# Optimization experiments

Measured on AMD Instinct MI355X. Metric: run time of the kernel, lower is better.

Reference implementation:

```python
import jax, jax.numpy as jnp
import numpy as np

B, T, C, H = 8, 2048, 256, 4
D = C // H  # head_dim = 64
SCALE = D ** -0.5


def setup_inputs() -> dict:
    key = jax.random.key(0)
    ks = jax.random.split(key, 5)
    return {
        "x": jax.random.normal(ks[0], (B, T, C), dtype=jnp.float32),
        "Wqkv": jax.random.normal(ks[1], (C, 3 * C), dtype=jnp.float32) * (C ** -0.5),
        "bqkv": jax.random.normal(ks[2], (3 * C,), dtype=jnp.float32) * 0.02,
        "Wproj": jax.random.normal(ks[3], (C, C), dtype=jnp.float32) * (C ** -0.5),
        "bproj": jax.random.normal(ks[4], (C,), dtype=jnp.float32) * 0.02,
    }


def reference(x, Wqkv, bqkv, Wproj, bproj):
    b, t, c = x.shape
    # QKV projection -> (3, B, H, T, D) matching torch permute(2,0,3,1,4)
    qkv = (x @ Wqkv + bqkv).reshape(b, t, 3, H, D)
    qkv = jnp.transpose(qkv, (2, 0, 3, 1, 4))
    q, k, v = qkv[0], qkv[1], qkv[2]  # each (B, H, T, D)
    # Full T x T scores (faithful to the original non-fused implementation)
    attn = jnp.einsum("bhqd,bhkd->bhqk", q, k) * SCALE
    causal = jnp.triu(jnp.ones((t, t), dtype=bool), k=1)  # True above diagonal
    attn = jnp.where(causal, -jnp.inf, attn)
    attn = jax.nn.softmax(attn, axis=-1)
    # dropout is identity in eval mode
    out = jnp.einsum("bhqk,bhkd->bhqd", attn, v)  # (B, H, T, D)
    out = jnp.transpose(out, (0, 2, 1, 3)).reshape(b, t, c)
    return out @ Wproj + bproj
```

## Files before the change

### kernel.cpp

```cpp
#include <hip/hip_runtime.h>
#include <hip/hip_bf16.h>
#include <math.h>

#define BATCH 8
#define SEQ   2048
#define CH    256
#define NH    4
#define HD    64
#define NQB   (SEQ / 64)
#define SCALE 0.125f

typedef short  bfrag __attribute__((ext_vector_type(8)));
typedef float  ffrag __attribute__((ext_vector_type(4)));
typedef unsigned short ushort_t;

__device__ __forceinline__ unsigned short f2bf(float f) {
    union { float f; unsigned int u; } v; v.f = f;
    unsigned int r = v.u + 0x7FFF + ((v.u >> 16) & 1);
    return (unsigned short)(r >> 16);
}

#define XN  (BATCH * SEQ * CH / 4)
#define WQN (CH * 3 * CH)
#define WPN (CH * CH)

__global__ __launch_bounds__(256) void prep_kernel(
    const float* __restrict__ x, const float* __restrict__ Wqkv,
    const float* __restrict__ Wproj,
    ushort_t* __restrict__ xb, ushort_t* __restrict__ WqkvT,
    ushort_t* __restrict__ WprojT) {
    const int fid = blockIdx.x * 256 + threadIdx.x;
    if (fid < XN) {
        const float4 v = ((const float4*)x)[fid];
        ushort4 p;
        p.x = f2bf(v.x); p.y = f2bf(v.y); p.z = f2bf(v.z); p.w = f2bf(v.w);
        ((ushort4*)xb)[fid] = p;
    } else if (fid < XN + WQN) {
        const int i = fid - XN;
        const int n = i >> 8, k = i & 255;
        WqkvT[n * CH + k] = f2bf(Wqkv[k * (3 * CH) + n]);
    } else if (fid < XN + WQN + WPN) {
        const int i = fid - XN - WQN;
        const int n = i >> 8, k = i & 255;
        WprojT[n * CH + k] = f2bf(Wproj[k * CH + n]);
    }
}

#define GLS 72

__global__ __launch_bounds__(256) void qkv_mfma_kernel(
    const ushort_t* __restrict__ xb, const ushort_t* __restrict__ Wt,
    const float* __restrict__ bias,
    ushort_t* __restrict__ Qb, ushort_t* __restrict__ Kb,
    ushort_t* __restrict__ Vtb) {
    __shared__ ushort_t smem[2 * 128 * GLS];
    ushort_t* As = smem;
    ushort_t* Bs = smem + 128 * GLS;

    const int tid = threadIdx.x;
    const int wv  = tid >> 6;
    const int ln  = tid & 63;
    const int l15 = ln & 15;
    const int l4  = ln >> 4;
    const int wr  = wv >> 1;
    const int wc  = wv & 1;
    const int n0  = blockIdx.x * 128;
    const int m0  = blockIdx.y * 128;

    ffrag acc[4][4];
    #pragma unroll
    for (int i = 0; i < 4; i++)
        #pragma unroll
        for (int j = 0; j < 4; j++) acc[i][j] = (ffrag){0.f, 0.f, 0.f, 0.f};

    for (int k0 = 0; k0 < CH; k0 += 64) {
        #pragma unroll
        for (int r = 0; r < 4; r++) {
            const int fid = tid + r * 256;
            const int row = fid >> 3, c8 = (fid & 7) * 8;
            *(uint4*)&As[row * GLS + c8] = *(const uint4*)&xb[(m0 + row) * CH + k0 + c8];
            *(uint4*)&Bs[row * GLS + c8] = *(const uint4*)&Wt[(n0 + row) * CH + k0 + c8];
        }
        __syncthreads();
        #pragma unroll
        for (int kk = 0; kk < 64; kk += 32) {
            bfrag a[4], b[4];
            #pragma unroll
            for (int i = 0; i < 4; i++)
                a[i] = *(const bfrag*)&As[(wr * 64 + i * 16 + l15) * GLS + kk + l4 * 8];
            #pragma unroll
            for (int j = 0; j < 4; j++)
                b[j] = *(const bfrag*)&Bs[(wc * 64 + j * 16 + l15) * GLS + kk + l4 * 8];
            #pragma unroll
            for (int i = 0; i < 4; i++)
                #pragma unroll
                for (int j = 0; j < 4; j++)
                    acc[i][j] = __builtin_amdgcn_mfma_f32_16x16x32_bf16(a[i], b[j], acc[i][j], 0, 0, 0);
        }
        __syncthreads();
    }

    const int mat = n0 >> 8;
    const int b   = m0 >> 11;
    if (mat < 2) {
        ushort_t* dst = (mat == 0) ? Qb : Kb;
        const float sc = (mat == 0) ? SCALE : 1.0f;
        #pragma unroll
        for (int j = 0; j < 4; j++) {
            const int n_glob = n0 + wc * 64 + j * 16 + l15;
            const int h = (n_glob >> 6) & 3;
            const int d = n_glob & 63;
            const float bj = bias[n_glob];
            const size_t rowbase = (size_t)((b * NH + h) * SEQ) * HD + d;
            #pragma unroll
            for (int i = 0; i < 4; i++) {
                const int t0 = (m0 & (SEQ - 1)) + wr * 64 + i * 16 + l4 * 4;
                #pragma unroll
                for (int r = 0; r < 4; r++)
                    dst[rowbase + (size_t)(t0 + r) * HD] = f2bf((acc[i][j][r] + bj) * sc);
            }
        }
    } else {
        ushort_t (*T)[136] = (ushort_t(*)[136])smem;
        #pragma unroll
        for (int j = 0; j < 4; j++) {
            const int n_local = wc * 64 + j * 16 + l15;
            const float bj = bias[n0 + n_local];
            #pragma unroll
            for (int i = 0; i < 4; i++) {
                const int m_base = wr * 64 + i * 16 + l4 * 4;
                ushort4 pk;
                pk.x = f2bf(acc[i][j][0] + bj);
                pk.y = f2bf(acc[i][j][1] + bj);
                pk.z = f2bf(acc[i][j][2] + bj);
                pk.w = f2bf(acc[i][j][3] + bj);
                *(ushort4*)&T[n_local][m_base] = pk;
            }
        }
        __syncthreads();
        const int t0 = m0 & (SEQ - 1);
        #pragma unroll
        for (int rr = 0; rr < 8; rr++) {
            const int fid = tid + rr * 256;
            const int row = fid >> 4;
            const int c8  = (fid & 15) * 8;
            const int n_glob = n0 + row;
            const int h = (n_glob >> 6) & 3;
            const int d = n_glob & 63;
            *(uint4*)&Vtb[(size_t)((b * NH + h) * HD + d) * SEQ + t0 + c8] =
                *(const uint4*)&T[row][c8];
        }
    }
}

#define LS 72

__global__ __launch_bounds__(256) void attn_mfma_kernel(
    const ushort_t* __restrict__ Qb, const ushort_t* __restrict__ Kb,
    const ushort_t* __restrict__ Vtb, ushort_t* __restrict__ out) {
    __shared__ ushort_t Qs[64][LS];
    __shared__ ushort_t Ks[64][LS];
    __shared__ ushort_t Vts[64][LS];
    __shared__ ushort_t Ps[4][16][LS];
    __shared__ float aw[4][16];
    __shared__ float lw[4][16];

    const int tid = threadIdx.x;
    const int wv  = tid >> 6;
    const int ln  = tid & 63;
    const int l15 = ln & 15;
    const int l4  = ln >> 4;

    const int L  = blockIdx.x;
    const int g  = L & 255;
    const int s4 = L >> 8;
    const int v  = g >> 5;
    const int qb = (s4 == 0) ? v : (s4 == 1) ? (15 - v) : (s4 == 2) ? (16 + v) : (31 - v);
    const int bh = g & 31;
    const int b  = bh >> 2;
    const int h  = bh & 3;

    {
        const ushort_t* Qp = Qb + (size_t)(bh * SEQ + qb * 64) * HD;
        #pragma unroll
        for (int r = 0; r < 2; r++) {
            const int fid = tid + r * 256;
            const int row = fid >> 3, c8 = (fid & 7) * 8;
            *(uint4*)&Qs[row][c8] = *(const uint4*)&Qp[row * HD + c8];
        }
    }
    __syncthreads();
    const bfrag bq0 = *(const bfrag*)&Qs[wv * 16 + l15][l4 * 8];
    const bfrag bq1 = *(const bfrag*)&Qs[wv * 16 + l15][32 + l4 * 8];

    ffrag o[4];
    #pragma unroll
    for (int n = 0; n < 4; n++) o[n] = (ffrag){0.f, 0.f, 0.f, 0.f};
    float m_q = -INFINITY;
    float l_q = 0.f;

    const int qg_l = qb * 64 + wv * 16 + l15;

    for (int kt = 0; kt <= qb; kt++) {
        {
            const ushort_t* Kp  = Kb  + (size_t)(bh * SEQ + kt * 64) * HD;
            const ushort_t* Vtp = Vtb + (size_t)(bh * HD) * SEQ + kt * 64;
            #pragma unroll
            for (int r = 0; r < 2; r++) {
                const int fid = tid + r * 256;
                const int row = fid >> 3, c8 = (fid & 7) * 8;
                *(uint4*)&Ks[row][c8]  = *(const uint4*)&Kp[row * HD + c8];
                *(uint4*)&Vts[row][c8] = *(const uint4*)&Vtp[row * SEQ + c8];
            }
        }
        __syncthreads();

        ffrag s[4];
        #pragma unroll
        for (int n = 0; n < 4; n++) {
            const bfrag ak0 = *(const bfrag*)&Ks[n * 16 + l15][l4 * 8];
            const bfrag ak1 = *(const bfrag*)&Ks[n * 16 + l15][32 + l4 * 8];
            ffrag z = (ffrag){0.f, 0.f, 0.f, 0.f};
            z = __builtin_amdgcn_mfma_f32_16x16x32_bf16(ak0, bq0, z, 0, 0, 0);
            z = __builtin_amdgcn_mfma_f32_16x16x32_bf16(ak1, bq1, z, 0, 0, 0);
            s[n] = z;
        }
        if (kt == qb) {
            #pragma unroll
            for (int n = 0; n < 4; n++)
                #pragma unroll
                for (int r = 0; r < 4; r++)
                    if (kt * 64 + n * 16 + l4 * 4 + r > qg_l) s[n][r] = -INFINITY;
        }

        float mx = s[0][0];
        #pragma unroll
        for (int n = 0; n < 4; n++)
            #pragma unroll
            for (int r = 0; r < 4; r++) mx = fmaxf(mx, s[n][r]);
        mx = fmaxf(mx, __shfl_xor(mx, 16));
        mx = fmaxf(mx, __shfl_xor(mx, 32));
        const float mo = m_q;
        const float mn = fmaxf(mo, mx);
        const float alpha = __expf(mo - mn);
        m_q = mn;

        float rs = 0.f;
        #pragma unroll
        for (int n = 0; n < 4; n++)
            #pragma unroll
            for (int r = 0; r < 4; r++) {
                const float p = __expf(s[n][r] - mn);
                s[n][r] = p;
                rs += p;
            }
        rs += __shfl_xor(rs, 16);
        rs += __shfl_xor(rs, 32);
        l_q = l_q * alpha + rs;

        if (l4 == 0) aw[wv][l15] = alpha;

        #pragma unroll
        for (int n = 0; n < 4; n++) {
            const __hip_bfloat162 pa = __float22bfloat162_rn(make_float2(s[n][0], s[n][1]));
            const __hip_bfloat162 pb = __float22bfloat162_rn(make_float2(s[n][2], s[n][3]));
            uint2 pk;
            pk.x = *(const unsigned int*)&pa;
            pk.y = *(const unsigned int*)&pb;
            *(uint2*)&Ps[wv][l15][n * 16 + l4 * 4] = pk;
        }

        const float4 al4 = *(const float4*)&aw[wv][l4 * 4];
        const float alr[4] = {al4.x, al4.y, al4.z, al4.w};
        #pragma unroll
        for (int n = 0; n < 4; n++)
            #pragma unroll
            for (int r = 0; r < 4; r++) o[n][r] *= alr[r];

        const bfrag ap0 = *(const bfrag*)&Ps[wv][l15][l4 * 8];
        const bfrag ap1 = *(const bfrag*)&Ps[wv][l15][32 + l4 * 8];
        #pragma unroll
        for (int n = 0; n < 4; n++) {
            const bfrag bv0 = *(const bfrag*)&Vts[n * 16 + l15][l4 * 8];
            const bfrag bv1 = *(const bfrag*)&Vts[n * 16 + l15][32 + l4 * 8];
            o[n] = __builtin_amdgcn_mfma_f32_16x16x32_bf16(ap0, bv0, o[n], 0, 0, 0);
            o[n] = __builtin_amdgcn_mfma_f32_16x16x32_bf16(ap1, bv1, o[n], 0, 0, 0);
        }
        __syncthreads();
    }

    if (l4 == 0) lw[wv][l15] = l_q;
    const float4 lv4 = *(const float4*)&lw[wv][l4 * 4];
    const float lvr[4] = {1.f / lv4.x, 1.f / lv4.y, 1.f / lv4.z, 1.f / lv4.w};
    const int tg = qb * 64 + wv * 16 + l4 * 4;
    ushort_t* op = out + (size_t)(b * SEQ) * CH + h * HD;
    #pragma unroll
    for (int n = 0; n < 4; n++)
        #pragma unroll
        for (int r = 0; r < 4; r++)
            op[(size_t)(tg + r) * CH + n * 16 + l15] = f2bf(o[n][r] * lvr[r]);
}

__global__ __launch_bounds__(256) void proj_mfma_kernel(
    const ushort_t* __restrict__ Ab, const ushort_t* __restrict__ Wt,
    const float* __restrict__ bias, float* __restrict__ O) {
    __shared__ ushort_t smem[2 * 128 * GLS];
    ushort_t* As = smem;
    ushort_t* Bs = smem + 128 * GLS;

    const int tid = threadIdx.x;
    const int wv  = tid >> 6;
    const int ln  = tid & 63;
    const int l15 = ln & 15;
    const int l4  = ln >> 4;
    const int wr  = wv >> 1;
    const int wc  = wv & 1;
    const int n0  = blockIdx.x * 128;
    const int m0  = blockIdx.y * 128;

    ffrag acc[4][4];
    #pragma unroll
    for (int i = 0; i < 4; i++)
        #pragma unroll
        for (int j = 0; j < 4; j++) acc[i][j] = (ffrag){0.f, 0.f, 0.f, 0.f};

    for (int k0 = 0; k0 < CH; k0 += 64) {
        #pragma unroll
        for (int r = 0; r < 4; r++) {
            const int fid = tid + r * 256;
            const int row = fid >> 3, c8 = (fid & 7) * 8;
            *(uint4*)&As[row * GLS + c8] = *(const uint4*)&Ab[(m0 + row) * CH + k0 + c8];
            *(uint4*)&Bs[row * GLS + c8] = *(const uint4*)&Wt[(n0 + row) * CH + k0 + c8];
        }
        __syncthreads();
        #pragma unroll
        for (int kk = 0; kk < 64; kk += 32) {
            bfrag a[4], b[4];
            #pragma unroll
            for (int i = 0; i < 4; i++)
                a[i] = *(const bfrag*)&As[(wr * 64 + i * 16 + l15) * GLS + kk + l4 * 8];
            #pragma unroll
            for (int j = 0; j < 4; j++)
                b[j] = *(const bfrag*)&Bs[(wc * 64 + j * 16 + l15) * GLS + kk + l4 * 8];
            #pragma unroll
            for (int i = 0; i < 4; i++)
                #pragma unroll
                for (int j = 0; j < 4; j++)
                    acc[i][j] = __builtin_amdgcn_mfma_f32_16x16x32_bf16(a[i], b[j], acc[i][j], 0, 0, 0);
        }
        __syncthreads();
    }

    #pragma unroll
    for (int j = 0; j < 4; j++) {
        const int n = n0 + wc * 64 + j * 16 + l15;
        const float bj = bias[n];
        #pragma unroll
        for (int i = 0; i < 4; i++) {
            const int m = m0 + wr * 64 + i * 16 + l4 * 4;
            #pragma unroll
            for (int r = 0; r < 4; r++)
                O[(size_t)(m + r) * CH + n] = acc[i][j][r] + bj;
        }
    }
}

extern "C" void kernel_launch(void* const* d_in, const int* in_sizes, int n_in,
                              void* d_out, int out_size, void* d_ws, size_t ws_size,
                              hipStream_t stream) {
    const float* x     = (const float*)d_in[0];
    const float* Wqkv  = (const float*)d_in[1];
    const float* bqkv  = (const float*)d_in[2];
    const float* Wproj = (const float*)d_in[3];
    const float* bproj = (const float*)d_in[4];
    float* out = (float*)d_out;

    const size_t BHTD = (size_t)BATCH * NH * SEQ * HD;
    ushort_t* xb     = (ushort_t*)d_ws;
    ushort_t* WqkvT  = xb + BHTD;
    ushort_t* WprojT = WqkvT + (size_t)3 * CH * CH;
    ushort_t* Qb     = WprojT + (size_t)CH * CH;
    ushort_t* Kb     = Qb + BHTD;
    ushort_t* Vtb    = Kb + BHTD;
    ushort_t* attn_b = Vtb + BHTD;

    const int M = BATCH * SEQ;

    {
        const int total = XN + WQN + WPN;
        prep_kernel<<<(total + 255) / 256, 256, 0, stream>>>(x, Wqkv, Wproj, xb, WqkvT, WprojT);
    }
    {
        dim3 grid((3 * CH) / 128, M / 128);
        qkv_mfma_kernel<<<grid, 256, 0, stream>>>(xb, WqkvT, bqkv, Qb, Kb, Vtb);
    }
    {
        attn_mfma_kernel<<<dim3(NQB * BATCH * NH), 256, 0, stream>>>(Qb, Kb, Vtb, attn_b);
    }
    {
        dim3 grid(CH / 128, M / 128);
        proj_mfma_kernel<<<grid, 256, 0, stream>>>(attn_b, WprojT, bproj, out);
    }
}
```

Baseline: 157.8 us.

## Prefetch K/V tiles into registers, fold log2e into Q scale, coalesce Q/K stores

The attention kernel now loads the next K/V tile into registers while it computes on the current one, so global load latency overlaps the MFMA work. The softmax uses exp2 with log2(e) folded into the Q scale, which removes a multiply per exponential. The P buffer reuses the Q shared tile, which cuts LDS use, and launch bounds ask for 5 blocks per SM. The QKV GEMM epilogue for Q and K goes through shared memory so it can write 16-byte coalesced stores, and the block schedule now starts with the longest query blocks first.

```diff
diff --git a/kernel.cpp b/kernel.cpp
--- a/kernel.cpp
+++ b/kernel.cpp
@@ -8,7 +8,7 @@
 #define NH    4
 #define HD    64
 #define NQB   (SEQ / 64)
-#define SCALE 0.125f
+#define QSCALE 0.18033688011112042f
 
 typedef short  bfrag __attribute__((ext_vector_type(8)));
 typedef float  ffrag __attribute__((ext_vector_type(4)));
@@ -102,26 +102,37 @@
 
     const int mat = n0 >> 8;
     const int b   = m0 >> 11;
+    const int t0  = m0 & (SEQ - 1);
+    ushort_t (*T)[136] = (ushort_t(*)[136])smem;
+
     if (mat < 2) {
+        const float sc = (mat == 0) ? QSCALE : 1.0f;
+        #pragma unroll
+        for (int j = 0; j < 4; j++) {
+            const int n_local = wc * 64 + j * 16 + l15;
+            const float bj = bias[n0 + n_local];
+            #pragma unroll
+            for (int i = 0; i < 4; i++) {
+                const int m_base = wr * 64 + i * 16 + l4 * 4;
+                #pragma unroll
+                for (int r = 0; r < 4; r++)
+                    T[m_base + r][n_local] = f2bf((acc[i][j][r] + bj) * sc);
+            }
+        }
+        __syncthreads();
         ushort_t* dst = (mat == 0) ? Qb : Kb;
-        const float sc = (mat == 0) ? SCALE : 1.0f;
-        #pragma unroll
-        for (int j = 0; j < 4; j++) {
-            const int n_glob = n0 + wc * 64 + j * 16 + l15;
+        #pragma unroll
+        for (int rr = 0; rr < 8; rr++) {
+            const int fid = tid + rr * 256;
+            const int row = fid >> 4;
+            const int c8  = (fid & 15) * 8;
+            const int n_glob = n0 + c8;
             const int h = (n_glob >> 6) & 3;
             const int d = n_glob & 63;
-            const float bj = bias[n_glob];
-            const size_t rowbase = (size_t)((b * NH + h) * SEQ) * HD + d;
-            #pragma unroll
-            for (int i = 0; i < 4; i++) {
-                const int t0 = (m0 & (SEQ - 1)) + wr * 64 + i * 16 + l4 * 4;
-                #pragma unroll
-                for (int r = 0; r < 4; r++)
-                    dst[rowbase + (size_t)(t0 + r) * HD] = f2bf((acc[i][j][r] + bj) * sc);
-            }
+            *(uint4*)&dst[((size_t)((b * NH + h) * SEQ) + t0 + row) * HD + d] =
+                *(const uint4*)&T[row][c8];
         }
     } else {
-        ushort_t (*T)[136] = (ushort_t(*)[136])smem;
         #pragma unroll
         for (int j = 0; j < 4; j++) {
             const int n_local = wc * 64 + j * 16 + l15;
@@ -138,7 +149,6 @@
             }
         }
         __syncthreads();
-        const int t0 = m0 & (SEQ - 1);
         #pragma unroll
         for (int rr = 0; rr < 8; rr++) {
             const int fid = tid + rr * 256;
@@ -153,15 +163,14 @@
     }
 }
 
-#define LS 72
-
-__global__ __launch_bounds__(256) void attn_mfma_kernel(
+#define LSA 72
+
+__global__ __launch_bounds__(256, 5) void attn_mfma_kernel(
     const ushort_t* __restrict__ Qb, const ushort_t* __restrict__ Kb,
     const ushort_t* __restrict__ Vtb, ushort_t* __restrict__ out) {
-    __shared__ ushort_t Qs[64][LS];
-    __shared__ ushort_t Ks[64][LS];
-    __shared__ ushort_t Vts[64][LS];
-    __shared__ ushort_t Ps[4][16][LS];
+    __shared__ ushort_t Qs[64][LSA];
+    __shared__ ushort_t Ks[64][LSA];
+    __shared__ ushort_t Vts[64][LSA];
     __shared__ float aw[4][16];
     __shared__ float lw[4][16];
 
@@ -175,7 +184,7 @@
     const int g  = L & 255;
     const int s4 = L >> 8;
     const int v  = g >> 5;
-    const int qb = (s4 == 0) ? v : (s4 == 1) ? (15 - v) : (s4 == 2) ? (16 + v) : (31 - v);
+    const int qb = (s4 == 0) ? (31 - v) : (s4 == 1) ? (16 + v) : (s4 == 2) ? (15 - v) : v;
     const int bh = g & 31;
     const int b  = bh >> 2;
     const int h  = bh & 3;
@@ -189,6 +198,17 @@
             *(uint4*)&Qs[row][c8] = *(const uint4*)&Qp[row * HD + c8];
         }
     }
+
+    const ushort_t* Kbase = Kb  + (size_t)bh * SEQ * HD;
+    const ushort_t* Vbase = Vtb + (size_t)bh * HD * SEQ;
+    const int srow = (tid + 0) >> 3,  sc8a = ((tid + 0) & 7) * 8;
+    const int srow2 = (tid + 256) >> 3, sc8b = ((tid + 256) & 7) * 8;
+    uint4 kK0, kK1, kV0, kV1;
+    kK0 = *(const uint4*)&Kbase[srow  * HD + sc8a];
+    kK1 = *(const uint4*)&Kbase[srow2 * HD + sc8b];
+    kV0 = *(const uint4*)&Vbase[srow  * SEQ + sc8a];
+    kV1 = *(const uint4*)&Vbase[srow2 * SEQ + sc8b];
+
     __syncthreads();
     const bfrag bq0 = *(const bfrag*)&Qs[wv * 16 + l15][l4 * 8];
     const bfrag bq1 = *(const bfrag*)&Qs[wv * 16 + l15][32 + l4 * 8];
@@ -202,18 +222,20 @@
     const int qg_l = qb * 64 + wv * 16 + l15;
 
     for (int kt = 0; kt <= qb; kt++) {
-        {
-            const ushort_t* Kp  = Kb  + (size_t)(bh * SEQ + kt * 64) * HD;
-            const ushort_t* Vtp = Vtb + (size_t)(bh * HD) * SEQ + kt * 64;
-            #pragma unroll
-            for (int r = 0; r < 2; r++) {
-                const int fid = tid + r * 256;
-                const int row = fid >> 3, c8 = (fid & 7) * 8;
-                *(uint4*)&Ks[row][c8]  = *(const uint4*)&Kp[row * HD + c8];
-                *(uint4*)&Vts[row][c8] = *(const uint4*)&Vtp[row * SEQ + c8];
-            }
-        }
-        __syncthreads();
+        *(uint4*)&Ks[srow][sc8a]   = kK0;
+        *(uint4*)&Ks[srow2][sc8b]  = kK1;
+        *(uint4*)&Vts[srow][sc8a]  = kV0;
+        *(uint4*)&Vts[srow2][sc8b] = kV1;
+        __syncthreads();
+
+        if (kt < qb) {
+            const ushort_t* Kp  = Kbase + (size_t)(kt + 1) * 64 * HD;
+            const ushort_t* Vtp = Vbase + (kt + 1) * 64;
+            kK0 = *(const uint4*)&Kp[srow  * HD + sc8a];
+            kK1 = *(const uint4*)&Kp[srow2 * HD + sc8b];
+            kV0 = *(const uint4*)&Vtp[srow  * SEQ + sc8a];
+            kV1 = *(const uint4*)&Vtp[srow2 * SEQ + sc8b];
+        }
 
         ffrag s[4];
         #pragma unroll
@@ -242,7 +264,7 @@
         mx = fmaxf(mx, __shfl_xor(mx, 32));
         const float mo = m_q;
         const float mn = fmaxf(mo, mx);
-        const float alpha = __expf(mo - mn);
+        const float alpha = __builtin_amdgcn_exp2f(mo - mn);
         m_q = mn;
 
         float rs = 0.f;
@@ -250,7 +272,7 @@
         for (int n = 0; n < 4; n++)
             #pragma unroll
             for (int r = 0; r < 4; r++) {
-                const float p = __expf(s[n][r] - mn);
+                const float p = __builtin_amdgcn_exp2f(s[n][r] - mn);
                 s[n][r] = p;
                 rs += p;
             }
@@ -267,7 +289,7 @@
             uint2 pk;
             pk.x = *(const unsigned int*)&pa;
             pk.y = *(const unsigned int*)&pb;
-            *(uint2*)&Ps[wv][l15][n * 16 + l4 * 4] = pk;
+            *(uint2*)&Qs[wv * 16 + l15][n * 16 + l4 * 4] = pk;
         }
 
         const float4 al4 = *(const float4*)&aw[wv][l4 * 4];
@@ -277,8 +299,8 @@
             #pragma unroll
             for (int r = 0; r < 4; r++) o[n][r] *= alr[r];
 
-        const bfrag ap0 = *(const bfrag*)&Ps[wv][l15][l4 * 8];
-        const bfrag ap1 = *(const bfrag*)&Ps[wv][l15][32 + l4 * 8];
+        const bfrag ap0 = *(const bfrag*)&Qs[wv * 16 + l15][l4 * 8];
+        const bfrag ap1 = *(const bfrag*)&Qs[wv * 16 + l15][32 + l4 * 8];
         #pragma unroll
         for (int n = 0; n < 4; n++) {
             const bfrag bv0 = *(const bfrag*)&Vts[n * 16 + l15][l4 * 8];
```

Measured after the change: 145.4 us. 1.09x faster.
